# Kernel optimization log

Measured on AMD Instinct MI355X. Metric: run time of the kernel, lower is better.

Reference implementation:

```python
import jax, jax.numpy as jnp
import numpy as np

B, N, D = 2048, 64, 128  # batch, num hist nodes (n-1), d_model
EPS = 1e-8


def setup_inputs() -> dict:
    key = jax.random.key(0)
    k1, k2, k3, k4, k5 = jax.random.split(key, 5)
    A_guide = jax.random.uniform(k1, (B, N, N), dtype=jnp.float32)  # nonneg for NMF
    X_guide = jax.random.normal(k2, (B, D, N), dtype=jnp.float32)
    x_new = jax.random.normal(k3, (B, 1, D), dtype=jnp.float32)
    U0 = jax.random.normal(k4, (B, N, N), dtype=jnp.float32)  # pre-softplus NMF init
    V0 = jax.random.normal(k5, (B, N, N), dtype=jnp.float32)
    return {"A_guide": A_guide, "X_guide": X_guide, "x_new": x_new, "U0": U0, "V0": V0}


def _nmf(A, U0, V0, n_iter=10):
    U = jax.nn.softplus(U0)
    V = jax.nn.softplus(V0)

    def step(carry, _):
        U, V = carry
        UT = jnp.swapaxes(U, 1, 2)
        V = V * (UT @ A) / (UT @ U @ V + EPS)
        VT = jnp.swapaxes(V, 1, 2)
        U = U * (A @ VT) / (U @ V @ VT + EPS)
        return (U, V), None

    (U, V), _ = jax.lax.scan(step, (U, V), None, length=n_iter)
    return U, V


def reference(A_guide, X_guide, x_new, U0, V0):
    d_model = X_guide.shape[1]
    n = X_guide.shape[2]
    # Step 1: deterministic NMF of historical adjacency
    U, V = _nmf(A_guide, U0, V0)
    # Step 2: orthogonal projection P = X X^T  (B, d, d)
    P = X_guide @ jnp.swapaxes(X_guide, 1, 2)
    # project new node feature: (B,1,d) @ (B,d,d) -> (B,d)
    x_p = (x_new @ P)[:, 0]
    # semantic attention: (B,1,n)
    attn_semantic = jnp.einsum('bd,bdn->bn', x_p, X_guide) / (d_model ** 0.5)
    # structural attention via UV reconstruction
    a = U @ V                                      # (B, n, n)
    x_p_rep = jnp.broadcast_to(x_p[:, None, :], (x_p.shape[0], n, x_p.shape[1]))
    x_p_UV = a @ x_p_rep                           # (B, n, d)
    attn_struct = x_p_UV @ X_guide                 # (B, n, n)
    fused = attn_semantic[:, None, :] * attn_struct  # broadcast (B,1,n)*(B,n,n)
    A_Tn = jax.nn.softmax(fused, axis=-1)
    return (A_Tn, x_p, U, V)
```

## Files before the change

### kernel.cpp

```cpp
#include <hip/hip_runtime.h>
#include <hip/hip_bf16.h>

#define EPS 1e-8f
#define LDH 72

typedef _Float16 half8 __attribute__((ext_vector_type(8)));
typedef _Float16 half4 __attribute__((ext_vector_type(4)));
typedef float f32x4 __attribute__((ext_vector_type(4)));

__device__ __forceinline__ float softplus_f(float x) {
    return fmaxf(x, 0.f) + log1pf(expf(-fabsf(x)));
}

struct Frag {
    half8 h0, h1;
};

__device__ __forceinline__ Frag load_frag(const _Float16* B, int i, int lr, int lk) {
    Frag f;
    f.h0 = *(const half8*)(B + (i * 16 + lr) * LDH + lk * 8);
    f.h1 = *(const half8*)(B + (i * 16 + lr) * LDH + 32 + lk * 8);
    return f;
}

__device__ __forceinline__ void mfma_acc(const Frag& a, const Frag& b, f32x4& acc) {
    acc = __builtin_amdgcn_mfma_f32_16x16x32_f16(a.h0, b.h0, acc, 0, 0, 0);
    acc = __builtin_amdgcn_mfma_f32_16x16x32_f16(a.h1, b.h1, acc, 0, 0, 0);
}

struct NmfLds {
    _Float16 U_rm[64 * LDH];
    _Float16 U_cm[64 * LDH];
    _Float16 V_rm[64 * LDH];
    _Float16 V_cm[64 * LDH];
    _Float16 WZ[64 * LDH];
    float vsum[64];
};

__global__ __launch_bounds__(256, 3) void nmf_kernel(const float* __restrict__ Ag,
                                                     const float* __restrict__ U0,
                                                     const float* __restrict__ V0,
                                                     float* __restrict__ out,
                                                     float* __restrict__ ws) {
    __shared__ NmfLds S;
    const int b = blockIdx.x;
    const int tid = threadIdx.x;
    const int wave = tid >> 6;
    const int lane = tid & 63;
    const int lr = lane & 15;
    const int lk = lane >> 4;

    const float* Ab = Ag + (size_t)b * 4096;
    const float* Ub = U0 + (size_t)b * 4096;
    const float* Vb = V0 + (size_t)b * 4096;

    float Ureg[4][4], Vreg[4][4];

#pragma unroll
    for (int t = 0; t < 4; ++t)
#pragma unroll
        for (int q = 0; q < 4; ++q) {
            const int r = wave * 16 + lk * 4 + q;
            const int c = t * 16 + lr;
            float a = Ab[r * 64 + c];
            S.WZ[r * LDH + c] = (_Float16)a;
            S.U_rm[c * LDH + r] = (_Float16)a;
        }
    __syncthreads();
    Frag af[4];
#pragma unroll
    for (int i = 0; i < 4; ++i) af[i] = load_frag(S.U_rm, i, lr, lk);
    Frag arm = load_frag(S.WZ, wave, lr, lk);
    __syncthreads();

#pragma unroll
    for (int t = 0; t < 4; ++t)
#pragma unroll
        for (int q = 0; q < 4; ++q) {
            const int r = wave * 16 + lk * 4 + q;
            const int c = t * 16 + lr;
            float u = softplus_f(Ub[r * 64 + c]);
            Ureg[t][q] = u;
            S.U_rm[r * LDH + c] = (_Float16)u;
            S.U_cm[c * LDH + r] = (_Float16)u;
            float v = softplus_f(Vb[r * 64 + c]);
            Vreg[t][q] = v;
            S.V_rm[r * LDH + c] = (_Float16)v;
            S.V_cm[c * LDH + r] = (_Float16)v;
        }
    __syncthreads();

    const f32x4 zero4 = {0.f, 0.f, 0.f, 0.f};

    for (int it = 0; it < 10; ++it) {
        Frag ucself = load_frag(S.U_cm, wave, lr, lk);
        Frag uf[4];
#pragma unroll
        for (int i = 0; i < 4; ++i) uf[i] = load_frag(S.U_cm, i, lr, lk);
        f32x4 T1[4] = {zero4, zero4, zero4, zero4};
        f32x4 W[4] = {zero4, zero4, zero4, zero4};
#pragma unroll
        for (int ct = 0; ct < 4; ++ct) {
            mfma_acc(ucself, af[ct], T1[ct]);
            mfma_acc(ucself, uf[ct], W[ct]);
        }
#pragma unroll
        for (int t = 0; t < 4; ++t) {
            half4 p = {(_Float16)W[t][0], (_Float16)W[t][1], (_Float16)W[t][2],
                       (_Float16)W[t][3]};
            *(half4*)(S.WZ + (t * 16 + lr) * LDH + wave * 16 + lk * 4) = p;
        }
        __syncthreads();

        Frag wf = load_frag(S.WZ, wave, lr, lk);
        Frag vcf[4];
#pragma unroll
        for (int i = 0; i < 4; ++i) vcf[i] = load_frag(S.V_cm, i, lr, lk);
        f32x4 WV[4] = {zero4, zero4, zero4, zero4};
#pragma unroll
        for (int ct = 0; ct < 4; ++ct) mfma_acc(wf, vcf[ct], WV[ct]);
        __syncthreads();

#pragma unroll
        for (int t = 0; t < 4; ++t) {
            half4 p;
#pragma unroll
            for (int q = 0; q < 4; ++q) {
                float v = Vreg[t][q] * T1[t][q] * __builtin_amdgcn_rcpf(WV[t][q] + EPS);
                Vreg[t][q] = v;
                _Float16 h = (_Float16)v;
                p[q] = h;
                S.V_rm[(wave * 16 + lk * 4 + q) * LDH + t * 16 + lr] = h;
            }
            *(half4*)(S.V_cm + (t * 16 + lr) * LDH + wave * 16 + lk * 4) = p;
        }
        __syncthreads();

        Frag vrself = load_frag(S.V_rm, wave, lr, lk);
        Frag vrf[4];
#pragma unroll
        for (int i = 0; i < 4; ++i) vrf[i] = load_frag(S.V_rm, i, lr, lk);
        f32x4 T2[4] = {zero4, zero4, zero4, zero4};
        f32x4 Y[4] = {zero4, zero4, zero4, zero4};
#pragma unroll
        for (int ct = 0; ct < 4; ++ct) {
            mfma_acc(arm, vrf[ct], T2[ct]);
            mfma_acc(vrself, vrf[ct], Y[ct]);
        }
#pragma unroll
        for (int t = 0; t < 4; ++t) {
            half4 p = {(_Float16)Y[t][0], (_Float16)Y[t][1], (_Float16)Y[t][2],
                       (_Float16)Y[t][3]};
            *(half4*)(S.WZ + (t * 16 + lr) * LDH + wave * 16 + lk * 4) = p;
        }
        __syncthreads();

        Frag urf = load_frag(S.U_rm, wave, lr, lk);
        Frag yf[4];
#pragma unroll
        for (int i = 0; i < 4; ++i) yf[i] = load_frag(S.WZ, i, lr, lk);
        f32x4 ZV[4] = {zero4, zero4, zero4, zero4};
#pragma unroll
        for (int ct = 0; ct < 4; ++ct) mfma_acc(urf, yf[ct], ZV[ct]);
#pragma unroll
        for (int t = 0; t < 4; ++t) {
            half4 p;
#pragma unroll
            for (int q = 0; q < 4; ++q) {
                float u = Ureg[t][q] * T2[t][q] * __builtin_amdgcn_rcpf(ZV[t][q] + EPS);
                Ureg[t][q] = u;
                _Float16 h = (_Float16)u;
                p[q] = h;
                S.U_rm[(wave * 16 + lk * 4 + q) * LDH + t * 16 + lr] = h;
            }
            *(half4*)(S.U_cm + (t * 16 + lr) * LDH + wave * 16 + lk * 4) = p;
        }
        __syncthreads();
    }

#pragma unroll
    for (int q = 0; q < 4; ++q) {
        float p = Vreg[0][q] + Vreg[1][q] + Vreg[2][q] + Vreg[3][q];
        p += __shfl_xor(p, 1);
        p += __shfl_xor(p, 2);
        p += __shfl_xor(p, 4);
        p += __shfl_xor(p, 8);
        if (lr == 0) S.vsum[wave * 16 + lk * 4 + q] = p;
    }
    __syncthreads();
#pragma unroll
    for (int q = 0; q < 4; ++q) {
        float p = 0.f;
#pragma unroll
        for (int t = 0; t < 4; ++t) p += Ureg[t][q] * S.vsum[t * 16 + lr];
        p += __shfl_xor(p, 1);
        p += __shfl_xor(p, 2);
        p += __shfl_xor(p, 4);
        p += __shfl_xor(p, 8);
        if (lr == 0) ws[(size_t)b * 64 + wave * 16 + lk * 4 + q] = p;
    }

    {
        float* Uout = out + 8650752 + (size_t)b * 4096;
        float* Vout = out + 17039360 + (size_t)b * 4096;
        const int rr = tid >> 2, qt = tid & 3;
        const _Float16* Up = S.U_rm + rr * LDH + qt * 16;
        const _Float16* Vp = S.V_rm + rr * LDH + qt * 16;
        half8 u0 = *(const half8*)(Up), u1 = *(const half8*)(Up + 8);
        half8 v0 = *(const half8*)(Vp), v1 = *(const half8*)(Vp + 8);
        float4* Uo = (float4*)(Uout + rr * 64 + qt * 16);
        float4* Vo = (float4*)(Vout + rr * 64 + qt * 16);
        Uo[0] = {(float)u0[0], (float)u0[1], (float)u0[2], (float)u0[3]};
        Uo[1] = {(float)u0[4], (float)u0[5], (float)u0[6], (float)u0[7]};
        Uo[2] = {(float)u1[0], (float)u1[1], (float)u1[2], (float)u1[3]};
        Uo[3] = {(float)u1[4], (float)u1[5], (float)u1[6], (float)u1[7]};
        Vo[0] = {(float)v0[0], (float)v0[1], (float)v0[2], (float)v0[3]};
        Vo[1] = {(float)v0[4], (float)v0[5], (float)v0[6], (float)v0[7]};
        Vo[2] = {(float)v1[0], (float)v1[1], (float)v1[2], (float)v1[3]};
        Vo[3] = {(float)v1[4], (float)v1[5], (float)v1[6], (float)v1[7]};
    }
}

__global__ __launch_bounds__(256) void xp_kernel(const float* __restrict__ Xg,
                                                 const float* __restrict__ xn,
                                                 float* __restrict__ out,
                                                 float* __restrict__ ws) {
    __shared__ float X[128 * 65];
    __shared__ float xnew[128];
    __shared__ float red[256];
    __shared__ float tbuf[64];
    __shared__ float xp[128];
    const int b = blockIdx.x, tid = threadIdx.x;
    const float* Xb = Xg + (size_t)b * 8192;

    for (int idx = tid; idx < 2048; idx += 256) {
        float4 v = ((const float4*)Xb)[idx];
        int d = idx >> 4, n = (idx * 4) & 63;
        X[d * 65 + n + 0] = v.x;
        X[d * 65 + n + 1] = v.y;
        X[d * 65 + n + 2] = v.z;
        X[d * 65 + n + 3] = v.w;
    }
    if (tid < 32) {
        float4 v = ((const float4*)(xn + (size_t)b * 128))[tid];
        xnew[tid * 4 + 0] = v.x;
        xnew[tid * 4 + 1] = v.y;
        xnew[tid * 4 + 2] = v.z;
        xnew[tid * 4 + 3] = v.w;
    }
    __syncthreads();
    {
        const int n = tid & 63, g = tid >> 6;
        float p = 0.f;
        for (int d = g * 32; d < g * 32 + 32; ++d) p += xnew[d] * X[d * 65 + n];
        red[g * 64 + n] = p;
    }
    __syncthreads();
    if (tid < 64) tbuf[tid] = red[tid] + red[64 + tid] + red[128 + tid] + red[192 + tid];
    __syncthreads();
    {
        const int d = tid & 127, h = tid >> 7;
        float p = 0.f;
        for (int n = h * 32; n < h * 32 + 32; ++n) p += X[d * 65 + n] * tbuf[n];
        red[h * 128 + d] = p;
    }
    __syncthreads();
    if (tid < 128) {
        float v = red[tid] + red[128 + tid];
        xp[tid] = v;
        out[8388608 + (size_t)b * 128 + tid] = v;
    }
    __syncthreads();
    {
        const int n = tid & 63, g = tid >> 6;
        float p = 0.f;
        for (int d = g * 32; d < g * 32 + 32; ++d) p += xp[d] * X[d * 65 + n];
        red[g * 64 + n] = p;
    }
    __syncthreads();
    if (tid < 64)
        ws[131072 + (size_t)b * 64 + tid] =
            red[tid] + red[64 + tid] + red[128 + tid] + red[192 + tid];
}

__global__ __launch_bounds__(256) void fuse_kernel(const float* __restrict__ ws,
                                                   float* __restrict__ out) {
    __shared__ float g[64];
    __shared__ float rs[64];
    __shared__ float gmax_s;
    const int b = blockIdx.x, tid = threadIdx.x;
    if (tid < 64) {
        float s = ws[131072 + (size_t)b * 64 + tid];
        g[tid] = s * s * 0.088388347648318447f;
        rs[tid] = ws[(size_t)b * 64 + tid];
    }
    __syncthreads();
    if (tid < 64) {
        float m = g[tid];
#pragma unroll
        for (int o = 1; o < 64; o <<= 1) m = fmaxf(m, __shfl_xor(m, o));
        if (tid == 0) gmax_s = m;
    }
    __syncthreads();
    const float gmax = gmax_s;
    const int i = tid >> 2, part = tid & 3;
    const float r = rs[i];
    float e[16];
    float sum = 0.f;
#pragma unroll
    for (int j = 0; j < 16; ++j) {
        e[j] = expf(r * (g[part * 16 + j] - gmax));
        sum += e[j];
    }
    sum += __shfl_xor(sum, 1);
    sum += __shfl_xor(sum, 2);
    const float inv = 1.f / sum;
    float* o = out + (size_t)b * 4096 + i * 64 + part * 16;
#pragma unroll
    for (int j = 0; j < 16; j += 4) {
        float4 v = {e[j] * inv, e[j + 1] * inv, e[j + 2] * inv, e[j + 3] * inv};
        ((float4*)o)[j >> 2] = v;
    }
}

extern "C" void kernel_launch(void* const* d_in, const int* in_sizes, int n_in,
                              void* d_out, int out_size, void* d_ws, size_t ws_size,
                              hipStream_t stream) {
    (void)in_sizes; (void)n_in; (void)out_size; (void)ws_size;
    const float* Ag = (const float*)d_in[0];
    const float* Xg = (const float*)d_in[1];
    const float* xn = (const float*)d_in[2];
    const float* U0 = (const float*)d_in[3];
    const float* V0 = (const float*)d_in[4];
    float* out = (float*)d_out;
    float* ws = (float*)d_ws;

    hipLaunchKernelGGL(nmf_kernel, dim3(2048), dim3(256), 0, stream, Ag, U0, V0, out, ws);
    hipLaunchKernelGGL(xp_kernel, dim3(2048), dim3(256), 0, stream, Xg, xn, out, ws);
    hipLaunchKernelGGL(fuse_kernel, dim3(2048), dim3(256), 0, stream, ws, out);
}
```

Measured before the change: 167.7 us.

## Swizzle NMF LDS tiles, compute V update transposed, raise occupancy to 4 blocks

Replaces the padded LDS layout (stride 72) with an XOR-swizzled unpadded 64-wide layout, shrinking shared memory so launch bounds can request 4 blocks per CU instead of 3. The V update is now computed in transposed orientation (V^T = V^T * (A^T U) / (W V)^T), which removes one barrier per iteration and the separate WV phase. Fragments are loaded per step inside the MFMA loops rather than preloaded into arrays, and the A fragment arrays are replaced by two fixed self fragments, lowering register pressure. The added index arithmetic and changed loop structure could offset the gains if occupancy is in fact limited by registers.

```diff
diff --git a/kernel.cpp b/kernel.cpp
--- a/kernel.cpp
+++ b/kernel.cpp
@@ -2,7 +2,6 @@
 #include <hip/hip_bf16.h>
 
 #define EPS 1e-8f
-#define LDH 72
 
 typedef _Float16 half8 __attribute__((ext_vector_type(8)));
 typedef _Float16 half4 __attribute__((ext_vector_type(4)));
@@ -12,14 +11,20 @@
     return fmaxf(x, 0.f) + log1pf(expf(-fabsf(x)));
 }
 
+__device__ __forceinline__ int swzh(int r, int c) {
+    return r * 64 + ((((c >> 3) ^ (r & 7)) << 3) | (c & 7));
+}
+
 struct Frag {
     half8 h0, h1;
 };
 
 __device__ __forceinline__ Frag load_frag(const _Float16* B, int i, int lr, int lk) {
+    const int row = i * 16 + lr;
+    const int x = lr & 7;
     Frag f;
-    f.h0 = *(const half8*)(B + (i * 16 + lr) * LDH + lk * 8);
-    f.h1 = *(const half8*)(B + (i * 16 + lr) * LDH + 32 + lk * 8);
+    f.h0 = *(const half8*)(B + row * 64 + ((lk ^ x) << 3));
+    f.h1 = *(const half8*)(B + row * 64 + (((lk + 4) ^ x) << 3));
     return f;
 }
 
@@ -29,15 +34,17 @@
 }
 
 struct NmfLds {
-    _Float16 U_rm[64 * LDH];
-    _Float16 U_cm[64 * LDH];
-    _Float16 V_rm[64 * LDH];
-    _Float16 V_cm[64 * LDH];
-    _Float16 WZ[64 * LDH];
-    float vsum[64];
+    _Float16 U_rm[4096];
+    _Float16 U_cm[4096];
+    _Float16 V_rm[4096];
+    _Float16 V_cm[4096];
+    union {
+        _Float16 WZ[4096];
+        float vp[4][64];
+    } u;
 };
 
-__global__ __launch_bounds__(256, 3) void nmf_kernel(const float* __restrict__ Ag,
+__global__ __launch_bounds__(256, 4) void nmf_kernel(const float* __restrict__ Ag,
                                                      const float* __restrict__ U0,
                                                      const float* __restrict__ V0,
                                                      float* __restrict__ out,
@@ -54,7 +61,8 @@
     const float* Ub = U0 + (size_t)b * 4096;
     const float* Vb = V0 + (size_t)b * 4096;
 
-    float Ureg[4][4], Vreg[4][4];
+    float Ureg[4][4];
+    float VregT[4][4];
 
 #pragma unroll
     for (int t = 0; t < 4; ++t)
@@ -63,14 +71,12 @@
             const int r = wave * 16 + lk * 4 + q;
             const int c = t * 16 + lr;
             float a = Ab[r * 64 + c];
-            S.WZ[r * LDH + c] = (_Float16)a;
-            S.U_rm[c * LDH + r] = (_Float16)a;
-        }
-    __syncthreads();
-    Frag af[4];
-#pragma unroll
-    for (int i = 0; i < 4; ++i) af[i] = load_frag(S.U_rm, i, lr, lk);
-    Frag arm = load_frag(S.WZ, wave, lr, lk);
+            S.U_rm[swzh(r, c)] = (_Float16)a;
+            S.U_cm[swzh(c, r)] = (_Float16)a;
+        }
+    __syncthreads();
+    const Frag arm = load_frag(S.U_rm, wave, lr, lk);
+    const Frag acm = load_frag(S.U_cm, wave, lr, lk);
     __syncthreads();
 
 #pragma unroll
@@ -79,14 +85,14 @@
         for (int q = 0; q < 4; ++q) {
             const int r = wave * 16 + lk * 4 + q;
             const int c = t * 16 + lr;
-            float u = softplus_f(Ub[r * 64 + c]);
-            Ureg[t][q] = u;
-            S.U_rm[r * LDH + c] = (_Float16)u;
-            S.U_cm[c * LDH + r] = (_Float16)u;
-            float v = softplus_f(Vb[r * 64 + c]);
-            Vreg[t][q] = v;
-            S.V_rm[r * LDH + c] = (_Float16)v;
-            S.V_cm[c * LDH + r] = (_Float16)v;
+            float uv = softplus_f(Ub[r * 64 + c]);
+            Ureg[t][q] = uv;
+            S.U_rm[swzh(r, c)] = (_Float16)uv;
+            S.U_cm[swzh(c, r)] = (_Float16)uv;
+            float vv = softplus_f(Vb[c * 64 + r]);
+            VregT[t][q] = vv;
+            S.V_cm[swzh(r, c)] = (_Float16)vv;
+            S.V_rm[swzh(c, r)] = (_Float16)vv;
         }
     __syncthreads();
 
@@ -94,74 +100,71 @@
 
     for (int it = 0; it < 10; ++it) {
         Frag ucself = load_frag(S.U_cm, wave, lr, lk);
-        Frag uf[4];
-#pragma unroll
-        for (int i = 0; i < 4; ++i) uf[i] = load_frag(S.U_cm, i, lr, lk);
-        f32x4 T1[4] = {zero4, zero4, zero4, zero4};
+        f32x4 T1T[4] = {zero4, zero4, zero4, zero4};
         f32x4 W[4] = {zero4, zero4, zero4, zero4};
 #pragma unroll
         for (int ct = 0; ct < 4; ++ct) {
-            mfma_acc(ucself, af[ct], T1[ct]);
-            mfma_acc(ucself, uf[ct], W[ct]);
+            Frag uct = load_frag(S.U_cm, ct, lr, lk);
+            mfma_acc(acm, uct, T1T[ct]);
+            mfma_acc(ucself, uct, W[ct]);
         }
 #pragma unroll
         for (int t = 0; t < 4; ++t) {
             half4 p = {(_Float16)W[t][0], (_Float16)W[t][1], (_Float16)W[t][2],
                        (_Float16)W[t][3]};
-            *(half4*)(S.WZ + (t * 16 + lr) * LDH + wave * 16 + lk * 4) = p;
+            *(half4*)(&S.u.WZ[swzh(t * 16 + lr, wave * 16 + lk * 4)]) = p;
         }
         __syncthreads();
 
-        Frag wf = load_frag(S.WZ, wave, lr, lk);
-        Frag vcf[4];
-#pragma unroll
-        for (int i = 0; i < 4; ++i) vcf[i] = load_frag(S.V_cm, i, lr, lk);
-        f32x4 WV[4] = {zero4, zero4, zero4, zero4};
-#pragma unroll
-        for (int ct = 0; ct < 4; ++ct) mfma_acc(wf, vcf[ct], WV[ct]);
-        __syncthreads();
+        Frag vtself = load_frag(S.V_cm, wave, lr, lk);
+        f32x4 WVT[4] = {zero4, zero4, zero4, zero4};
+#pragma unroll
+        for (int ct = 0; ct < 4; ++ct) {
+            Frag wct = load_frag(S.u.WZ, ct, lr, lk);
+            mfma_acc(vtself, wct, WVT[ct]);
+        }
 
 #pragma unroll
         for (int t = 0; t < 4; ++t) {
             half4 p;
 #pragma unroll
             for (int q = 0; q < 4; ++q) {
-                float v = Vreg[t][q] * T1[t][q] * __builtin_amdgcn_rcpf(WV[t][q] + EPS);
-                Vreg[t][q] = v;
+                float v =
+                    VregT[t][q] * T1T[t][q] * __builtin_amdgcn_rcpf(WVT[t][q] + EPS);
+                VregT[t][q] = v;
                 _Float16 h = (_Float16)v;
                 p[q] = h;
-                S.V_rm[(wave * 16 + lk * 4 + q) * LDH + t * 16 + lr] = h;
+                S.V_cm[swzh(wave * 16 + lk * 4 + q, t * 16 + lr)] = h;
             }
-            *(half4*)(S.V_cm + (t * 16 + lr) * LDH + wave * 16 + lk * 4) = p;
+            *(half4*)(&S.V_rm[swzh(t * 16 + lr, wave * 16 + lk * 4)]) = p;
         }
         __syncthreads();
 
         Frag vrself = load_frag(S.V_rm, wave, lr, lk);
-        Frag vrf[4];
-#pragma unroll
-        for (int i = 0; i < 4; ++i) vrf[i] = load_frag(S.V_rm, i, lr, lk);
         f32x4 T2[4] = {zero4, zero4, zero4, zero4};
         f32x4 Y[4] = {zero4, zero4, zero4, zero4};
 #pragma unroll
         for (int ct = 0; ct < 4; ++ct) {
-            mfma_acc(arm, vrf[ct], T2[ct]);
-            mfma_acc(vrself, vrf[ct], Y[ct]);
+            Frag vct = load_frag(S.V_rm, ct, lr, lk);
+            mfma_acc(arm, vct, T2[ct]);
+            mfma_acc(vrself, vct, Y[ct]);
         }
 #pragma unroll
         for (int t = 0; t < 4; ++t) {
             half4 p = {(_Float16)Y[t][0], (_Float16)Y[t][1], (_Float16)Y[t][2],
                        (_Float16)Y[t][3]};
-            *(half4*)(S.WZ + (t * 16 + lr) * LDH + wave * 16 + lk * 4) = p;
+            *(half4*)(&S.u.WZ[swzh(t * 16 + lr, wave * 16 + lk * 4)]) = p;
         }
         __syncthreads();
 
-        Frag urf = load_frag(S.U_rm, wave, lr, lk);
-        Frag yf[4];
-#pragma unroll
-        for (int i = 0; i < 4; ++i) yf[i] = load_frag(S.WZ, i, lr, lk);
+        Frag urself = load_frag(S.U_rm, wave, lr, lk);
         f32x4 ZV[4] = {zero4, zero4, zero4, zero4};
 #pragma unroll
-        for (int ct = 0; ct < 4; ++ct) mfma_acc(urf, yf[ct], ZV[ct]);
+        for (int ct = 0; ct < 4; ++ct) {
+            Frag yct = load_frag(S.u.WZ, ct, lr, lk);
+            mfma_acc(urself, yct, ZV[ct]);
+        }
+
 #pragma unroll
         for (int t = 0; t < 4; ++t) {
             half4 p;
@@ -171,28 +174,37 @@
                 Ureg[t][q] = u;
                 _Float16 h = (_Float16)u;
                 p[q] = h;
-                S.U_rm[(wave * 16 + lk * 4 + q) * LDH + t * 16 + lr] = h;
+                S.U_rm[swzh(wave * 16 + lk * 4 + q, t * 16 + lr)] = h;
             }
-            *(half4*)(S.U_cm + (t * 16 + lr) * LDH + wave * 16 + lk * 4) = p;
+            *(half4*)(&S.U_cm[swzh(t * 16 + lr, wave * 16 + lk * 4)]) = p;
         }
         __syncthreads();
     }
 
-#pragma unroll
-    for (int q = 0; q < 4; ++q) {
-        float p = Vreg[0][q] + Vreg[1][q] + Vreg[2][q] + Vreg[3][q];
-        p += __shfl_xor(p, 1);
-        p += __shfl_xor(p, 2);
-        p += __shfl_xor(p, 4);
-        p += __shfl_xor(p, 8);
-        if (lr == 0) S.vsum[wave * 16 + lk * 4 + q] = p;
+    {
+        float part[4];
+#pragma unroll
+        for (int t = 0; t < 4; ++t) {
+            float s = VregT[t][0] + VregT[t][1] + VregT[t][2] + VregT[t][3];
+            s += __shfl_xor(s, 16);
+            s += __shfl_xor(s, 32);
+            part[t] = s;
+        }
+        if (lk == 0) {
+#pragma unroll
+            for (int t = 0; t < 4; ++t) S.u.vp[wave][t * 16 + lr] = part[t];
+        }
     }
     __syncthreads();
 #pragma unroll
     for (int q = 0; q < 4; ++q) {
         float p = 0.f;
 #pragma unroll
-        for (int t = 0; t < 4; ++t) p += Ureg[t][q] * S.vsum[t * 16 + lr];
+        for (int t = 0; t < 4; ++t) {
+            float vs = S.u.vp[0][t * 16 + lr] + S.u.vp[1][t * 16 + lr] +
+                       S.u.vp[2][t * 16 + lr] + S.u.vp[3][t * 16 + lr];
+            p += Ureg[t][q] * vs;
+        }
         p += __shfl_xor(p, 1);
         p += __shfl_xor(p, 2);
         p += __shfl_xor(p, 4);
@@ -204,10 +216,12 @@
         float* Uout = out + 8650752 + (size_t)b * 4096;
         float* Vout = out + 17039360 + (size_t)b * 4096;
         const int rr = tid >> 2, qt = tid & 3;
-        const _Float16* Up = S.U_rm + rr * LDH + qt * 16;
-        const _Float16* Vp = S.V_rm + rr * LDH + qt * 16;
-        half8 u0 = *(const half8*)(Up), u1 = *(const half8*)(Up + 8);
-        half8 v0 = *(const half8*)(Vp), v1 = *(const half8*)(Vp + 8);
+        const _Float16* Up = S.U_rm + swzh(rr, qt * 16);
+        const _Float16* Vp = S.V_rm + swzh(rr, qt * 16);
+        half8 u0 = *(const half8*)(Up);
+        half8 u1 = *(const half8*)(S.U_rm + swzh(rr, qt * 16 + 8));
+        half8 v0 = *(const half8*)(Vp);
+        half8 v1 = *(const half8*)(S.V_rm + swzh(rr, qt * 16 + 8));
         float4* Uo = (float4*)(Uout + rr * 64 + qt * 16);
         float4* Vo = (float4*)(Vout + rr * 64 + qt * 16);
         Uo[0] = {(float)u0[0], (float)u0[1], (float)u0[2], (float)u0[3]};
```

Result: faster. 159.3 us (-5.0%).
